# Kernel tuning notes

Measured on AMD Instinct MI355X. Metric: run time of the kernel, lower is better.

## Reference

```python
import jax, jax.numpy as jnp
import numpy as np
import math

MODEL_DIM = 1024
BATCH = 4
SEQ = 4096
ATTENTION_INPUT = 'both'


def make_F(model_dim, attention_input):
    F = jnp.zeros((model_dim, model_dim), dtype=jnp.float32)
    if attention_input == 'both':
        a = model_dim
    else:
        a = model_dim // 2
    # faithful to source: elif means 'both' only hits the first branch
    if attention_input in ['both', 'only_sem']:
        idx = jnp.arange(0, a)
        F = F.at[idx, idx].set(1.0)
    elif attention_input in ['only_pos']:
        idx = jnp.arange(a, 2 * a)
        F = F.at[idx, idx].set(1.0)
    return F


def setup_inputs() -> dict:
    key = jax.random.key(0)
    kx, kq, kk, kv = jax.random.split(key, 4)
    x = jax.random.normal(kx, (BATCH, SEQ, MODEL_DIM), dtype=jnp.float32)
    Q = jax.random.normal(kq, (MODEL_DIM, MODEL_DIM), dtype=jnp.float32) / math.sqrt(MODEL_DIM)
    K = jax.random.normal(kk, (MODEL_DIM, MODEL_DIM), dtype=jnp.float32) / math.sqrt(MODEL_DIM)
    V = jax.random.normal(kv, (MODEL_DIM, MODEL_DIM), dtype=jnp.float32) / math.sqrt(MODEL_DIM)
    return {"x": x, "Q": Q, "K": K, "V": V}


def reference(x, Q, K, V):
    model_dim = Q.shape[0]
    F = make_F(model_dim, ATTENTION_INPUT)
    Qx = x @ F @ Q            # [B, S, D]
    Kx = x @ F @ K            # [B, S, D]
    Vx = x @ V                # [B, S, D]
    scores = jnp.einsum('bqd,bkd->bqk', Qx, Kx) / math.sqrt(model_dim)  # [B, S, S]
    seq = x.shape[1]
    causal_mask = jnp.triu(jnp.ones((seq, seq), dtype=bool), k=1)       # True above diagonal
    scores = jnp.where(causal_mask, -jnp.inf, scores)
    probs = jax.nn.softmax(scores, axis=-1)
    return jnp.einsum('bqk,bkd->bqd', probs, Vx)
```

## Files before the change

### kernel.cpp

```cpp
#include <hip/hip_runtime.h>
#include <cstdint>
#include <cstddef>
#include <cmath>


typedef unsigned short u16;
typedef __bf16  bf16x8 __attribute__((ext_vector_type(8)));
typedef float   f32x4  __attribute__((ext_vector_type(4)));
typedef unsigned short u16x4 __attribute__((ext_vector_type(4)));

typedef __attribute__((address_space(1))) void gvoid;
typedef __attribute__((address_space(3))) void lvoid;

__device__ __forceinline__ u16 f2bf(float f) {
  union { float f; unsigned u; } v; v.f = f;
  unsigned u = v.u;
  u += 0x7FFFu + ((u >> 16) & 1u);
  return (u16)(u >> 16);
}
__device__ __forceinline__ float bf2f(u16 h) {
  union { unsigned u; float f; } v; v.u = ((unsigned)h) << 16;
  return v.f;
}
__device__ __forceinline__ void async16(const void* g, void* l) {
  __builtin_amdgcn_global_load_lds((gvoid*)(void*)g, (lvoid*)l, 16, 0, 0);
}

__global__ void __launch_bounds__(256) cvt_f32_bf16(const float4* __restrict__ in,
                                                    u16* __restrict__ out, int n4) {
  int i = blockIdx.x * 256 + threadIdx.x;
  if (i >= n4) return;
  float4 v = in[i];
  u16x4 o = { f2bf(v.x), f2bf(v.y), f2bf(v.z), f2bf(v.w) };
  *(u16x4*)(out + 4 * (size_t)i) = o;
}

__device__ __forceinline__ u16 to_bfs(float v, float s) { return f2bf(v * s); }
__device__ __forceinline__ u16 to_bfs(u16 v, float)     { return v; }

template <typename TIN>
__global__ void __launch_bounds__(256) transpose_to_bf16(
    const TIN* __restrict__ in, u16* __restrict__ out,
    int rows, int cols, long inStride, long outStride, float scale) {
  __shared__ u16 t[64][68];
  int rt = blockIdx.x * 64, ct = blockIdx.y * 64;
  long ib = (long)blockIdx.z * inStride, ob = (long)blockIdx.z * outStride;
  int tx = threadIdx.x & 63, ty = threadIdx.x >> 6;
#pragma unroll
  for (int r = ty; r < 64; r += 4)
    t[r][tx] = to_bfs(in[ib + (long)(rt + r) * cols + ct + tx], scale);
  __syncthreads();
#pragma unroll
  for (int r = ty; r < 64; r += 4)
    out[ob + (long)(ct + r) * rows + rt + tx] = t[tx][r];
}

template <bool OUTF32, bool TRI, bool CK, int BM>
__global__ void __launch_bounds__(256, BM == 256 ? 2 : 4) gemm_bt(
    const u16* __restrict__ A, const u16* __restrict__ Bt, void* __restrict__ C,
    int K, int lda, int ldb, int ldc,
    long aStride, long bStride, long cStride, float alpha) {
  constexpr int MR = BM / 32;
  constexpr int AQ = BM / 64;
  int mt, nt, bz;
  if (TRI) {
    const int bid = blockIdx.x;
    int m = (int)((sqrtf(4.0f * (float)bid + 1.0f) - 1.0f) * 0.5f);
    while ((m + 1) * (m + 2) <= bid) ++m;
    while (m * (m + 1) > bid) --m;
    mt = m; nt = bid - m * (m + 1);
    bz = blockIdx.z;
  } else if (CK) {
    const int id = blockIdx.x;
    const int g = id & 7, mid = (id >> 3) & 31, hi = id >> 8;
    bz = mid & 3; nt = mid >> 2;
    mt = (hi == 0) ? 31 - g : (hi == 1) ? 16 + g : (hi == 2) ? 15 - g : g;
  } else {
    mt = blockIdx.x; nt = blockIdx.y; bz = blockIdx.z;
  }
  const int tid = threadIdx.x, wv = tid >> 6, ln = tid & 63;
  const u16* Ag = A + (long)bz * aStride + (long)(mt * BM) * lda;
  const u16* Bg = Bt + (long)bz * bStride + (long)(nt * 128) * ldb;

  __shared__ __align__(16) __bf16 As[2][BM * 32];
  __shared__ __align__(16) __bf16 Bs[2][128 * 32];

  f32x4 acc[MR][4];
#pragma unroll
  for (int i = 0; i < MR; ++i)
#pragma unroll
    for (int j = 0; j < 4; ++j)
#pragma unroll
      for (int r = 0; r < 4; ++r) acc[i][j][r] = 0.f;

  const int kend = CK ? (((mt + 1) * BM < K) ? (mt + 1) * BM : K) : K;
  const int wm = wv & 1, wn = wv >> 1;
  const int mrow = wm * (BM / 2), nrow = wn * 64;
  const int lr = ln & 15, quad = ln >> 4;

  long aOff[AQ]; int aLds[AQ];
#pragma unroll
  for (int q = 0; q < AQ; ++q) {
    int c = q * 256 + tid, row = c >> 2, c8i = c & 3;
    aOff[q] = (long)row * lda + ((c8i ^ ((row >> 1) & 3)) << 3);
    aLds[q] = c * 8;
  }
  long bOff[2]; int bLds[2];
#pragma unroll
  for (int q = 0; q < 2; ++q) {
    int c = q * 256 + tid, row = c >> 2, c8i = c & 3;
    bOff[q] = (long)row * ldb + ((c8i ^ ((row >> 1) & 3)) << 3);
    bLds[q] = c * 8;
  }
  const int swq = (quad ^ ((lr >> 1) & 3)) << 3;

  for (int k0 = 0; k0 < kend; k0 += 64) {
#pragma unroll
    for (int p = 0; p < 2; ++p) {
      const long kk = k0 + p * 32;
#pragma unroll
      for (int q = 0; q < AQ; ++q)
        async16(Ag + kk + aOff[q], (char*)As[p] + aLds[q] * 2);
#pragma unroll
      for (int q = 0; q < 2; ++q)
        async16(Bg + kk + bOff[q], (char*)Bs[p] + bLds[q] * 2);
    }
    __syncthreads();
#pragma unroll
    for (int p = 0; p < 2; ++p) {
      bf16x8 af[MR], bfr[4];
#pragma unroll
      for (int u = 0; u < MR; ++u)
        af[u] = *(const bf16x8*)&As[p][(mrow + u * 16 + lr) * 32 + swq];
#pragma unroll
      for (int j = 0; j < 4; ++j)
        bfr[j] = *(const bf16x8*)&Bs[p][(nrow + j * 16 + lr) * 32 + swq];
#pragma unroll
      for (int u = 0; u < MR; ++u)
#pragma unroll
        for (int j = 0; j < 4; ++j)
          acc[u][j] = __builtin_amdgcn_mfma_f32_16x16x32_bf16(af[u], bfr[j], acc[u][j], 0, 0, 0);
    }
    __syncthreads();
  }

  const long cb = (long)bz * cStride;
#pragma unroll
  for (int i = 0; i < MR; ++i) {
    int row0 = mt * BM + mrow + i * 16 + quad * 4;
#pragma unroll
    for (int j = 0; j < 4; ++j) {
      int col = nt * 128 + nrow + j * 16 + lr;
#pragma unroll
      for (int r = 0; r < 4; ++r) {
        float v = acc[i][j][r] * alpha;
        long idx = cb + (long)(row0 + r) * ldc + col;
        if (OUTF32) ((float*)C)[idx] = v;
        else        ((u16*)C)[idx]  = f2bf(v);
      }
    }
  }
}

__global__ void __launch_bounds__(256) softmax_rows(u16* __restrict__ Sb,
                                                    long bStride, int S) {
  const int row = blockIdx.x;
  u16* p = Sb + (long)blockIdx.y * bStride + (long)row * S;
  const int L = row + 1;
  const int Lpad = (L + 255) & ~255;
  const int tid = threadIdx.x, ln = tid & 63, wv = tid >> 6;
  __shared__ float red[8];

  float vals[16];
  float lmax = -3.4e38f;
#pragma unroll
  for (int k = 0; k < 16; ++k) {
    int j = tid + k * 256;
    if (j < L) { float v = bf2f(p[j]); vals[k] = v; lmax = fmaxf(lmax, v); }
  }
#pragma unroll
  for (int o = 32; o > 0; o >>= 1) lmax = fmaxf(lmax, __shfl_down(lmax, o));
  if (ln == 0) red[wv] = lmax;
  __syncthreads();
  float m = fmaxf(fmaxf(red[0], red[1]), fmaxf(red[2], red[3]));

  float lsum = 0.f;
#pragma unroll
  for (int k = 0; k < 16; ++k) {
    int j = tid + k * 256;
    if (j < L) { float e = __expf(vals[k] - m); vals[k] = e; lsum += e; }
  }
#pragma unroll
  for (int o = 32; o > 0; o >>= 1) lsum += __shfl_down(lsum, o);
  __syncthreads();
  if (ln == 0) red[wv] = lsum;
  __syncthreads();
  float inv = 1.f / (red[0] + red[1] + red[2] + red[3]);
#pragma unroll
  for (int k = 0; k < 16; ++k) {
    int j = tid + k * 256;
    if (j < L) p[j] = f2bf(vals[k] * inv);
  }
  for (int j = L + tid; j < Lpad; j += 256) p[j] = 0;
}

extern "C" void kernel_launch(void* const* d_in, const int* in_sizes, int n_in,
                              void* d_out, int out_size, void* d_ws, size_t ws_size,
                              hipStream_t stream) {
  const float* x = (const float*)d_in[0];
  const float* Q = (const float*)d_in[1];
  const float* K = (const float*)d_in[2];
  const float* V = (const float*)d_in[3];
  float* out = (float*)d_out;

  constexpr int  Bb = 4, S = 4096, D = 1024;
  constexpr long MB = 1024 * 1024;
  if (ws_size < (size_t)(224 * MB)) return;

  char* ws = (char*)d_ws;
  u16* QKx  = (u16*)(ws);
  u16* Vxt  = (u16*)(ws + 64 * MB);
  u16* Sb   = (u16*)(ws + 96 * MB);
  u16* Vtmp = (u16*)(ws + 96 * MB);
  u16* XB   = (u16*)(ws + 128 * MB);
  u16* WTqk = (u16*)(ws + 160 * MB);
  u16* WTv  = (u16*)(ws + 164 * MB);

  const long SD = (long)S * D, SS = (long)S * S;

  cvt_f32_bf16<<<dim3((Bb * S * D / 4) / 256), 256, 0, stream>>>(
      (const float4*)x, XB, Bb * S * D / 4);

  transpose_to_bf16<float><<<dim3(16, 16, 1), 256, 0, stream>>>(
      Q, WTqk, 1024, 1024, 0, 0, 0.03125f);
  transpose_to_bf16<float><<<dim3(16, 16, 1), 256, 0, stream>>>(
      K, WTqk + 1024 * 1024, 1024, 1024, 0, 0, 1.0f);
  transpose_to_bf16<float><<<dim3(16, 16, 1), 256, 0, stream>>>(
      V, WTv, 1024, 1024, 0, 0, 1.0f);

  gemm_bt<false, false, false, 256><<<dim3(64, 16, 1), 256, 0, stream>>>(
      XB, WTqk, QKx, 1024, 1024, 1024, 2048, 0, 0, 0, 1.0f);
  gemm_bt<false, false, false, 256><<<dim3(64, 8, 1), 256, 0, stream>>>(
      XB, WTv, Vtmp, 1024, 1024, 1024, 1024, 0, 0, 0, 1.0f);

  transpose_to_bf16<u16><<<dim3(64, 16, Bb), 256, 0, stream>>>(
      Vtmp, Vxt, S, D, SD, SD, 1.0f);

  gemm_bt<false, true, false, 256><<<dim3(272, 1, Bb), 256, 0, stream>>>(
      QKx, QKx + 1024, Sb, 1024, 2048, 2048, S, 2 * SD, 2 * SD, SS, 1.0f);

  softmax_rows<<<dim3(S, Bb), 256, 0, stream>>>(Sb, SS, S);

  gemm_bt<true, false, true, 128><<<dim3(1024, 1, 1), 256, 0, stream>>>(
      Sb, Vxt, out, S, S, S, D, SS, SD, SD, 1.0f);
}
```

Measured before the change: 504.9 us.

## Add 256x256 8-wave GEMM with interleaved async prefetch for projections and scores

Adds a new 512-thread GEMM kernel with 256x256 output tiles and a double-buffered LDS pipeline. It interleaves async global-to-LDS loads for the next k-tile with MFMA chunks, using fine-grained barriers, vmcnt waits and setprio. The QK/V projections and the causal score GEMM now use it, which doubles the tile width and halves the block count. This aims to raise data reuse per block and hide load latency behind compute, at the cost of more registers and LDS per block and coarser triangular tiles near the diagonal.

```diff
diff --git a/kernel.cpp b/kernel.cpp
--- a/kernel.cpp
+++ b/kernel.cpp
@@ -53,6 +53,126 @@
 #pragma unroll
   for (int r = ty; r < 64; r += 4)
     out[ob + (long)(ct + r) * rows + rt + tx] = t[tx][r];
+}
+
+
+#define G8_BAR()  __builtin_amdgcn_s_barrier()
+#define G8_VMC4() asm volatile("s_waitcnt vmcnt(4)" ::: "memory")
+#define G8_VMC0() asm volatile("s_waitcnt vmcnt(0)" ::: "memory")
+
+#define G8_STAGE_A(bn, kp, kb) do { \
+    async16(Ag + (kb) + a0, (void*)&As[bn][kp][l0]); \
+    async16(Ag + (kb) + a1, (void*)&As[bn][kp][l1]); } while (0)
+#define G8_STAGE_B(bn, kp, kb) do { \
+    async16(Bg + (kb) + b0, (void*)&Bs[bn][kp][l0]); \
+    async16(Bg + (kb) + b1, (void*)&Bs[bn][kp][l1]); } while (0)
+
+#define G8_LDA(bc, kp, ch) do { _Pragma("unroll") \
+    for (int u_ = 0; u_ < 4; ++u_) \
+      af[u_] = *(const bf16x8*)&As[bc][kp][(wm * 128 + (ch) * 64 + u_ * 16 + lr) * 32 + swq]; \
+  } while (0)
+#define G8_LDB(bc, kp) do { _Pragma("unroll") \
+    for (int j_ = 0; j_ < 4; ++j_) \
+      bf[j_] = *(const bf16x8*)&Bs[bc][kp][(wn * 64 + j_ * 16 + lr) * 32 + swq]; \
+  } while (0)
+
+#define G8_MFMA(ch) do { \
+    __builtin_amdgcn_s_setprio(1); \
+    _Pragma("unroll") for (int u_ = 0; u_ < 4; ++u_) \
+      _Pragma("unroll") for (int j_ = 0; j_ < 4; ++j_) \
+        acc[(ch) * 4 + u_][j_] = __builtin_amdgcn_mfma_f32_16x16x32_bf16( \
+            af[u_], bf[j_], acc[(ch) * 4 + u_][j_], 0, 0, 0); \
+    __builtin_amdgcn_s_setprio(0); } while (0)
+
+#define G8_TILE(bc, bn, kt, kn) do { \
+    bf16x8 af[4], bf[4]; \
+     \
+    G8_LDB(bc, 0); G8_LDA(bc, 0, 0); \
+    G8_STAGE_A(bn, 0, (kn)); \
+    G8_BAR(); G8_MFMA(0); G8_BAR(); \
+     \
+    G8_LDA(bc, 0, 1); \
+    G8_STAGE_B(bn, 0, (kn)); \
+    G8_BAR(); G8_MFMA(1); G8_VMC4(); G8_BAR(); \
+     \
+    G8_LDB(bc, 1); G8_LDA(bc, 1, 0); \
+    G8_STAGE_A(bn, 1, (kn) + 32); \
+    G8_BAR(); G8_MFMA(0); G8_BAR(); \
+     \
+    G8_LDA(bc, 1, 1); \
+    G8_STAGE_B(bn, 1, (kn) + 32); \
+    G8_BAR(); G8_MFMA(1); G8_VMC4(); G8_BAR(); } while (0)
+
+template <bool OUTF32, bool TRI>
+__global__ void __launch_bounds__(512, 2) gemm8_bt(
+    const u16* __restrict__ A, const u16* __restrict__ Bt, void* __restrict__ C,
+    int K, int lda, int ldb, int ldc,
+    long aStride, long bStride, long cStride, float alpha) {
+  int mt, nt;
+  if (TRI) {
+    const int bid = blockIdx.x;
+    int m = (int)((sqrtf(8.0f * (float)bid + 1.0f) - 1.0f) * 0.5f);
+    while ((m + 1) * (m + 2) / 2 <= bid) ++m;
+    while (m * (m + 1) / 2 > bid) --m;
+    mt = m; nt = bid - m * (m + 1) / 2;
+  } else { mt = blockIdx.x; nt = blockIdx.y; }
+  const int bz = blockIdx.z;
+  const int tid = threadIdx.x, wv = tid >> 6, ln = tid & 63;
+  const int wm = wv & 1, wn = wv >> 1;
+  const int lr = ln & 15, quad = ln >> 4;
+  const int swq = (quad ^ ((lr >> 1) & 3)) << 3;
+  const u16* Ag = A + (long)bz * aStride + (long)(mt * 256) * lda;
+  const u16* Bg = Bt + (long)bz * bStride + (long)(nt * 256) * ldb;
+
+  __shared__ __align__(16) __bf16 As[2][2][256 * 32];
+  __shared__ __align__(16) __bf16 Bs[2][2][256 * 32];
+
+  f32x4 acc[8][4];
+#pragma unroll
+  for (int i = 0; i < 8; ++i)
+#pragma unroll
+    for (int j = 0; j < 4; ++j)
+#pragma unroll
+      for (int r = 0; r < 4; ++r) acc[i][j][r] = 0.f;
+
+  const int c0 = tid, c1 = tid + 512;
+  const int r0 = c0 >> 2, r1 = c1 >> 2;
+  const long a0 = (long)r0 * lda + (((c0 & 3) ^ ((r0 >> 1) & 3)) << 3);
+  const long a1 = (long)r1 * lda + (((c1 & 3) ^ ((r1 >> 1) & 3)) << 3);
+  const long b0 = (long)r0 * ldb + (((c0 & 3) ^ ((r0 >> 1) & 3)) << 3);
+  const long b1 = (long)r1 * ldb + (((c1 & 3) ^ ((r1 >> 1) & 3)) << 3);
+  const int l0 = c0 * 8, l1 = c1 * 8;
+
+  const int kend = K;
+
+  G8_STAGE_A(0, 0, 0); G8_STAGE_B(0, 0, 0);
+  G8_STAGE_A(0, 1, 32); G8_STAGE_B(0, 1, 32);
+  G8_VMC4(); G8_BAR();
+
+  for (int k0 = 0; k0 < kend; k0 += 128) {
+    const long kn0 = (k0 + 64  < kend) ? (long)k0 + 64  : (long)k0;
+    const long kn1 = (k0 + 128 < kend) ? (long)k0 + 128 : (long)k0 + 64;
+    G8_TILE(0, 1, k0, kn0);
+    G8_TILE(1, 0, k0 + 64, kn1);
+  }
+  G8_VMC0();
+
+  const long cb = (long)bz * cStride;
+#pragma unroll
+  for (int i = 0; i < 8; ++i) {
+    int row0 = mt * 256 + wm * 128 + i * 16 + quad * 4;
+#pragma unroll
+    for (int j = 0; j < 4; ++j) {
+      int col = nt * 256 + wn * 64 + j * 16 + lr;
+#pragma unroll
+      for (int r = 0; r < 4; ++r) {
+        float v = acc[i][j][r] * alpha;
+        long idx = cb + (long)(row0 + r) * ldc + col;
+        if (OUTF32) ((float*)C)[idx] = v;
+        else        ((u16*)C)[idx]  = f2bf(v);
+      }
+    }
+  }
 }
 
 template <bool OUTF32, bool TRI, bool CK, int BM>
@@ -238,15 +358,15 @@
   transpose_to_bf16<float><<<dim3(16, 16, 1), 256, 0, stream>>>(
       V, WTv, 1024, 1024, 0, 0, 1.0f);
 
-  gemm_bt<false, false, false, 256><<<dim3(64, 16, 1), 256, 0, stream>>>(
+  gemm8_bt<false, false><<<dim3(64, 8, 1), 512, 0, stream>>>(
       XB, WTqk, QKx, 1024, 1024, 1024, 2048, 0, 0, 0, 1.0f);
-  gemm_bt<false, false, false, 256><<<dim3(64, 8, 1), 256, 0, stream>>>(
+  gemm8_bt<false, false><<<dim3(64, 4, 1), 512, 0, stream>>>(
       XB, WTv, Vtmp, 1024, 1024, 1024, 1024, 0, 0, 0, 1.0f);
 
   transpose_to_bf16<u16><<<dim3(64, 16, Bb), 256, 0, stream>>>(
       Vtmp, Vxt, S, D, SD, SD, 1.0f);
 
-  gemm_bt<false, true, false, 256><<<dim3(272, 1, Bb), 256, 0, stream>>>(
+  gemm8_bt<false, true><<<dim3(136, 1, Bb), 512, 0, stream>>>(
       QKx, QKx + 1024, Sb, 1024, 2048, 2048, S, 2 * SD, 2 * SD, SS, 1.0f);
 
   softmax_rows<<<dim3(S, Bb), 256, 0, stream>>>(Sb, SS, S);
```

Result: no change. 505.6 us (+0.1%).
